# Kernel tuning notes

Measured on AMD Instinct MI355X. Metric: run time of the kernel, lower is better.

Reference implementation:

```python
import jax, jax.numpy as jnp
import numpy as np

DIM = 256
HEADS = 8
HEAD_DIM = DIM // HEADS
SR = 2
SCALE = HEAD_DIM ** -0.5
EPS = 1e-5
DN = ('NCHW', 'OIHW', 'NCHW')


def setup_inputs() -> dict:
    key = jax.random.key(0)
    ks = jax.random.split(key, 8)
    B, H, W = 4, 64, 64
    x = jax.random.normal(ks[0], (B, H * W, DIM), dtype=jnp.float32)
    # depthwise 3x3 convs (groups=dim): kernel [out_ch, 1, 3, 3]
    to_q_w = jax.random.normal(ks[1], (DIM, 1, 3, 3), dtype=jnp.float32) * 0.1
    to_kv_w = jax.random.normal(ks[2], (2 * DIM, 1, 3, 3), dtype=jnp.float32) * 0.1
    # spatial-reduction conv: kernel=stride=SR, with bias (torch Conv2d default)
    sr_w = jax.random.normal(ks[3], (DIM, DIM, SR, SR), dtype=jnp.float32) * 0.02
    sr_b = jax.random.normal(ks[4], (DIM,), dtype=jnp.float32) * 0.01
    ln_g = jnp.ones((DIM,), dtype=jnp.float32)
    ln_b = jnp.zeros((DIM,), dtype=jnp.float32)
    proj_w = jax.random.normal(ks[5], (DIM, DIM), dtype=jnp.float32) * 0.02
    proj_b = jax.random.normal(ks[6], (DIM,), dtype=jnp.float32) * 0.01
    return {
        'x': x, 'to_q_w': to_q_w, 'to_kv_w': to_kv_w,
        'sr_w': sr_w, 'sr_b': sr_b, 'ln_g': ln_g, 'ln_b': ln_b,
        'proj_w': proj_w, 'proj_b': proj_b, 'H': H, 'W': W,
    }


def reference(x, to_q_w, to_kv_w, sr_w, sr_b, ln_g, ln_b, proj_w, proj_b, H, W):
    B, N, C = x.shape
    x_nchw = x.reshape(B, H, W, C).transpose(0, 3, 1, 2)  # [B,C,H,W]

    # depthwise-conv Q projection (padding=1, stride=1 -> SAME)
    q = jax.lax.conv_general_dilated(x_nchw, to_q_w, (1, 1), 'SAME',
                                     feature_group_count=C, dimension_numbers=DN)
    q = q.transpose(0, 2, 3, 1).reshape(B, N, HEADS, HEAD_DIM).transpose(0, 2, 1, 3)  # [B,h,N,d]

    # spatial reduction: strided conv (kernel=stride=SR, no padding) + LayerNorm
    xr = jax.lax.conv_general_dilated(x_nchw, sr_w, (SR, SR), 'VALID',
                                      dimension_numbers=DN) + sr_b[None, :, None, None]
    Hs, Ws = xr.shape[2], xr.shape[3]
    Nk = Hs * Ws
    xr = xr.reshape(B, C, Nk).transpose(0, 2, 1)  # [B,Nk,C]
    mu = xr.mean(axis=-1, keepdims=True)
    var = ((xr - mu) ** 2).mean(axis=-1, keepdims=True)
    xr = (xr - mu) / jnp.sqrt(var + EPS) * ln_g + ln_b
    xr = xr.reshape(B, Hs, Ws, C).transpose(0, 3, 1, 2)  # [B,C,Hs,Ws]

    # depthwise-conv KV projection; torch group-major channel order out_ch=2*g+j
    kv = jax.lax.conv_general_dilated(xr, to_kv_w, (1, 1), 'SAME',
                                      feature_group_count=C, dimension_numbers=DN)
    kv = kv.transpose(0, 2, 3, 1).reshape(B, Nk, 2, HEADS, HEAD_DIM).transpose(2, 0, 3, 1, 4)
    k, v = kv[0], kv[1]  # [B,h,Nk,d]

    attn = jax.nn.softmax(jnp.einsum('bhqd,bhkd->bhqk', q, k) * SCALE, axis=-1)
    out = jnp.einsum('bhqk,bhkd->bhqd', attn, v)  # [B,h,N,d]
    out = out.transpose(0, 2, 1, 3).reshape(B, N, C)
    return out @ proj_w.T + proj_b
```

## Files before the change

kernel.cpp:

```cpp
#include <hip/hip_runtime.h>
#include <stdint.h>

typedef unsigned short u16;
typedef short s16x8 __attribute__((ext_vector_type(8)));
typedef short s16x4 __attribute__((ext_vector_type(4)));
typedef float f32x4 __attribute__((ext_vector_type(4)));
typedef uint32_t u32x4 __attribute__((ext_vector_type(4)));

#define SCALE 0.17677669529663689f
#define LOG2E 1.4426950408889634f
#define QS (SCALE * LOG2E)
#define EPS 1e-5f

static __device__ __forceinline__ float b2f(u16 u){
  union { uint32_t i; float f; } cv; cv.i = ((uint32_t)u) << 16; return cv.f;
}
static __device__ __forceinline__ u16 f2b(float f){
  uint32_t u = __float_as_uint(f);
  uint32_t r = (u + 0x7FFFu + ((u >> 16) & 1u)) >> 16;
  return (u16)r;
}
static __device__ __forceinline__ uint32_t cvtpk(float lo, float hi){
  uint32_t r;
  asm("v_cvt_pk_bf16_f32 %0, %1, %2" : "=v"(r) : "v"(lo), "v"(hi));
  return r;
}

__global__ __launch_bounds__(256) void k_prep(const float* __restrict__ x,
                                              const float* __restrict__ srw,
                                              const float* __restrict__ pw,
                                              u16* __restrict__ xbf,
                                              u16* __restrict__ wsr,
                                              u16* __restrict__ wpj){
  const int t = blockIdx.x*256 + threadIdx.x;
  if (t < 1048576){
    const float4 xv = ((const float4*)x)[t];
    ushort4 o;
    o.x = f2b(xv.x); o.y = f2b(xv.y); o.z = f2b(xv.z); o.w = f2b(xv.w);
    ((ushort4*)xbf)[t] = o;
  } else if (t < 1310720){
    const int t2 = t - 1048576;
    const int co = t2 >> 10, k = t2 & 1023;
    const float v = srw[(co<<10) + ((k&255)<<2) + (k>>8)];
    wsr[((((k>>3)<<8) + co)<<3) + (k&7)] = f2b(v);
  } else {
    const int t3 = t - 1310720;
    const int co = t3 >> 8, k = t3 & 255;
    wpj[((((k>>3)<<8) + co)<<3) + (k&7)] = f2b(pw[(co<<8) + k]);
  }
}

__global__ __launch_bounds__(256) void k_qconv(const u16* __restrict__ xbf,
                                               const float* __restrict__ w,
                                               u16* __restrict__ q){
  const int c = threadIdx.x;
  const int blk = blockIdx.x;
  const int b = blk >> 9;
  const int y = (blk >> 3) & 63;
  const int x0 = (blk & 7) << 3;
  float wv[9];
#pragma unroll
  for (int t = 0; t < 9; ++t) wv[t] = w[c*9 + t];
  float xin[3][10];
#pragma unroll
  for (int r = 0; r < 3; ++r){
    const int yy = y + r - 1;
    const bool yok = (unsigned)yy < 64u;
#pragma unroll
    for (int j = 0; j < 10; ++j){
      const int xx = x0 + j - 1;
      const bool ok = yok && ((unsigned)xx < 64u);
      xin[r][j] = ok ? b2f(xbf[(((b<<12) + (yy<<6) + xx) << 8) + c]) : 0.f;
    }
  }
#pragma unroll
  for (int j = 0; j < 8; ++j){
    float acc = 0.f;
#pragma unroll
    for (int r = 0; r < 3; ++r)
#pragma unroll
      for (int t = 0; t < 3; ++t)
        acc += xin[r][j+t] * wv[r*3 + t];
    q[(((b<<12) + (y<<6) + x0 + j) << 8) + c] = f2b(acc * QS);
  }
}

__global__ __launch_bounds__(256) void k_srgemm(const u16* __restrict__ xbf,
                                                const u16* __restrict__ wsr,
                                                const float* __restrict__ srb,
                                                const float* __restrict__ lng,
                                                const float* __restrict__ lnb,
                                                float* __restrict__ lnxr){
  __shared__ float red_s[16][4], red_q[16][4];
  __shared__ float mu_s[16], rs_s[16];
  const int tid = threadIdx.x;
  const int l = tid & 63, w = tid >> 6;
  const int r15 = l & 15, g = l >> 4;
  const int m0 = blockIdx.x << 4;
  const int ma = m0 + r15;
  const int bb_ = ma >> 10, nk = ma & 1023;
  const int hs = nk >> 5, wsx = nk & 31;
  int pixbase[4];
#pragma unroll
  for (int p = 0; p < 4; ++p){
    const int y = 2*hs + (p>>1), xx = 2*wsx + (p&1);
    pixbase[p] = (((bb_<<12) + (y<<6) + xx) << 8);
  }
  f32x4 acc[4];
#pragma unroll
  for (int i = 0; i < 4; ++i) acc[i] = (f32x4){0.f,0.f,0.f,0.f};
  for (int ks = 0; ks < 32; ++ks){
    const s16x8 af = *reinterpret_cast<const s16x8*>(
        xbf + pixbase[ks>>3] + ((ks&7)<<5) + (g<<3));
#pragma unroll
    for (int i = 0; i < 4; ++i){
      const int co = (((w<<2)+i)<<4) + r15;
      const s16x8 bf = *reinterpret_cast<const s16x8*>(
          wsr + (((((ks<<2)+g)<<8) + co)<<3));
      acc[i] = __builtin_amdgcn_mfma_f32_16x16x32_bf16(af, bf, acc[i], 0, 0, 0);
    }
  }
  float gv[4], bv[4];
#pragma unroll
  for (int i = 0; i < 4; ++i){
    const int co = (((w<<2)+i)<<4) + r15;
    const float sb = srb[co];
    gv[i] = lng[co]; bv[i] = lnb[co];
#pragma unroll
    for (int r = 0; r < 4; ++r) acc[i][r] += sb;
  }
  float s_r[4], q_r[4];
#pragma unroll
  for (int r = 0; r < 4; ++r){
    float s = 0.f, qq = 0.f;
#pragma unroll
    for (int i = 0; i < 4; ++i){ const float v = acc[i][r]; s += v; qq += v*v; }
#pragma unroll
    for (int off = 1; off < 16; off <<= 1){
      s  += __shfl_xor(s, off);
      qq += __shfl_xor(qq, off);
    }
    s_r[r] = s; q_r[r] = qq;
  }
  if (r15 == 0){
#pragma unroll
    for (int r = 0; r < 4; ++r){
      red_s[(g<<2)+r][w] = s_r[r];
      red_q[(g<<2)+r][w] = q_r[r];
    }
  }
  __syncthreads();
  if (tid < 16){
    const float s  = red_s[tid][0]+red_s[tid][1]+red_s[tid][2]+red_s[tid][3];
    const float qq = red_q[tid][0]+red_q[tid][1]+red_q[tid][2]+red_q[tid][3];
    const float mu = s * (1.f/256.f);
    mu_s[tid] = mu;
    rs_s[tid] = rsqrtf(qq*(1.f/256.f) - mu*mu + EPS);
  }
  __syncthreads();
  float mur[4], rsr[4];
#pragma unroll
  for (int r = 0; r < 4; ++r){ mur[r] = mu_s[(g<<2)+r]; rsr[r] = rs_s[(g<<2)+r]; }
#pragma unroll
  for (int i = 0; i < 4; ++i){
    const int co = (((w<<2)+i)<<4) + r15;
#pragma unroll
    for (int r = 0; r < 4; ++r)
      lnxr[(m0+(g<<2)+r)*256 + co] = (acc[i][r]-mur[r])*rsr[r]*gv[i] + bv[i];
  }
}

__global__ __launch_bounds__(512) void k_kvconv(const float* __restrict__ lnxr,
                                                const float* __restrict__ w,
                                                u16* __restrict__ kbuf,
                                                u16* __restrict__ vT){
  const int o = threadIdx.x;
  const int blk = blockIdx.x;
  const int b = blk >> 7;
  const int y = (blk >> 2) & 31;
  const int x0 = (blk & 3) << 3;
  const int g = o >> 1;
  float wv[9];
#pragma unroll
  for (int t = 0; t < 9; ++t) wv[t] = w[o*9 + t];
  float xin[3][10];
#pragma unroll
  for (int r = 0; r < 3; ++r){
    const int yy = y + r - 1;
    const bool yok = (unsigned)yy < 32u;
#pragma unroll
    for (int j = 0; j < 10; ++j){
      const int xx = x0 + j - 1;
      const bool ok = yok && ((unsigned)xx < 32u);
      xin[r][j] = ok ? lnxr[(((b<<10) + (yy<<5) + xx) << 8) + g] : 0.f;
    }
  }
  float acc[8];
#pragma unroll
  for (int j = 0; j < 8; ++j){
    float a = 0.f;
#pragma unroll
    for (int r = 0; r < 3; ++r)
#pragma unroll
      for (int t = 0; t < 3; ++t)
        a += xin[r][j+t] * wv[r*3 + t];
    acc[j] = a;
  }
  const int t = o & 255;
  const int h = t >> 5, dd = t & 31;
  if (o < 256){
    const int nkbase = (((b<<3) + h) << 10) + (y<<5) + x0;
#pragma unroll
    for (int j = 0; j < 8; ++j)
      kbuf[((nkbase + j) << 5) + dd] = f2b(acc[j]);
  } else {
    s16x8 pack;
#pragma unroll
    for (int j = 0; j < 8; ++j) pack[j] = (short)f2b(acc[j]);
    const int col0 = (y<<5) + x0;
    const int colS = (((col0>>3) ^ (dd&7)) << 3);
    *reinterpret_cast<s16x8*>(
        vT + (((((b<<3) + h) << 5) + dd) << 10) + colS) = pack;
  }
}

__global__ __launch_bounds__(512) void k_attn(const u16* __restrict__ q,
                                              const u16* __restrict__ kbuf,
                                              const u16* __restrict__ vT,
                                              u16* __restrict__ attb){
  __shared__ __align__(16) u16 KL[32768];
  __shared__ __align__(16) u16 VL[32768];
  const int tid = threadIdx.x;
  const int l = tid & 63, w = tid >> 6;
  const int i = blockIdx.x;
  const int xcd = i & 7, slot = i >> 3;
  const int bh = (xcd<<2) + (slot>>3);
  const int chunk = slot & 7;
  const int b = bh >> 3, h = bh & 7;
  const int r15 = l & 15, g = l >> 4;
  const int n0 = (chunk<<9) + (w<<6);

  {
    const uint4* kg = (const uint4*)(kbuf + (bh<<15));
    const uint4* vg = (const uint4*)(vT   + (bh<<15));
    uint4* kl = (uint4*)KL;
    uint4* vl = (uint4*)VL;
#pragma unroll
    for (int r = 0; r < 8; ++r){
      kl[(r<<9) + tid] = kg[(r<<9) + tid];
      vl[(r<<9) + tid] = vg[(r<<9) + tid];
    }
  }
  __syncthreads();

  s16x8 qf[4];
#pragma unroll
  for (int qi = 0; qi < 4; ++qi)
    qf[qi] = *reinterpret_cast<const s16x8*>(
        q + (((b<<12) + n0 + (qi<<4) + r15) << 8) + (h<<5) + (g<<3));

  f32x4 acc[4][2];
#pragma unroll
  for (int qi = 0; qi < 4; ++qi){
    acc[qi][0] = (f32x4){0.f,0.f,0.f,0.f};
    acc[qi][1] = (f32x4){0.f,0.f,0.f,0.f};
  }
  const f32x4 zero = {0.f,0.f,0.f,0.f};
  float lsum[4] = {0.f,0.f,0.f,0.f};
  const int vswz = (r15 & 7);

  for (int kv0 = 0; kv0 < 1024; kv0 += 64){
    s16x8 kf[4];
#pragma unroll
    for (int st = 0; st < 4; ++st)
      kf[st] = *reinterpret_cast<const s16x8*>(
          KL + ((kv0 + (st<<4) + r15) << 5) + (g<<3));
    s16x8 vf[2][2];
#pragma unroll
    for (int pr = 0; pr < 2; ++pr)
#pragma unroll
      for (int h2 = 0; h2 < 2; ++h2){
        const int cl  = kv0 + (pr<<5) + (g<<2);
        const int cl2 = cl + 16;
        const int rb  = ((h2<<4) + r15) << 10;
        const s16x4 v0 = *reinterpret_cast<const s16x4*>(
            VL + rb + (((cl >>3) ^ vswz) << 3) + (cl &7));
        const s16x4 v1 = *reinterpret_cast<const s16x4*>(
            VL + rb + (((cl2>>3) ^ vswz) << 3) + (cl2&7));
        s16x8 vv;
        vv[0]=v0[0]; vv[1]=v0[1]; vv[2]=v0[2]; vv[3]=v0[3];
        vv[4]=v1[0]; vv[5]=v1[1]; vv[6]=v1[2]; vv[7]=v1[3];
        vf[pr][h2] = vv;
      }
#pragma unroll
    for (int qi = 0; qi < 4; ++qi){
      f32x4 s[4];
      __builtin_amdgcn_s_setprio(1);
#pragma unroll
      for (int st = 0; st < 4; ++st)
        s[st] = __builtin_amdgcn_mfma_f32_16x16x32_bf16(kf[st], qf[qi], zero, 0, 0, 0);
      __builtin_amdgcn_s_setprio(0);
      float p[4][4];
      float ps = 0.f;
#pragma unroll
      for (int st = 0; st < 4; ++st)
#pragma unroll
        for (int r = 0; r < 4; ++r){
          const float e = __builtin_amdgcn_exp2f(s[st][r]);
          p[st][r] = e;
          ps += e;
        }
      ps += __shfl_xor(ps, 16);
      ps += __shfl_xor(ps, 32);
      lsum[qi] += ps;
      const u32x4 pk0 = {cvtpk(p[0][0],p[0][1]), cvtpk(p[0][2],p[0][3]),
                         cvtpk(p[1][0],p[1][1]), cvtpk(p[1][2],p[1][3])};
      const u32x4 pk1 = {cvtpk(p[2][0],p[2][1]), cvtpk(p[2][2],p[2][3]),
                         cvtpk(p[3][0],p[3][1]), cvtpk(p[3][2],p[3][3])};
      const s16x8 pf0 = __builtin_bit_cast(s16x8, pk0);
      const s16x8 pf1 = __builtin_bit_cast(s16x8, pk1);
      __builtin_amdgcn_s_setprio(1);
#pragma unroll
      for (int h2 = 0; h2 < 2; ++h2){
        acc[qi][h2] = __builtin_amdgcn_mfma_f32_16x16x32_bf16(pf0, vf[0][h2], acc[qi][h2], 0, 0, 0);
        acc[qi][h2] = __builtin_amdgcn_mfma_f32_16x16x32_bf16(pf1, vf[1][h2], acc[qi][h2], 0, 0, 0);
      }
      __builtin_amdgcn_s_setprio(0);
    }
  }
#pragma unroll
  for (int qi = 0; qi < 4; ++qi){
    const float linv = 1.f / lsum[qi];
#pragma unroll
    for (int r = 0; r < 4; ++r){
      const float fl = __shfl(linv, (g<<2) + r);
      const int n = n0 + (qi<<4) + (g<<2) + r;
      u16* orow = attb + (((b<<12) + n) << 8) + (h<<5) + r15;
      orow[0]  = f2b(acc[qi][0][r] * fl);
      orow[16] = f2b(acc[qi][1][r] * fl);
    }
  }
}

__global__ __launch_bounds__(256) void k_proj(const u16* __restrict__ attb,
                                              const u16* __restrict__ wpj,
                                              const float* __restrict__ pb,
                                              float* __restrict__ out){
  const int tid = threadIdx.x;
  const int l = tid & 63, w = tid >> 6;
  const int r15 = l & 15, g = l >> 4;
  const int m0 = blockIdx.x << 4;
  f32x4 acc[4];
#pragma unroll
  for (int i = 0; i < 4; ++i) acc[i] = (f32x4){0.f,0.f,0.f,0.f};
  const u16* arow = attb + (m0 + r15)*256 + (g<<3);
#pragma unroll
  for (int ks = 0; ks < 8; ++ks){
    const s16x8 af = *reinterpret_cast<const s16x8*>(arow + (ks<<5));
#pragma unroll
    for (int i = 0; i < 4; ++i){
      const int co = (((w<<2)+i)<<4) + r15;
      const s16x8 bf = *reinterpret_cast<const s16x8*>(
          wpj + (((((ks<<2)+g)<<8) + co)<<3));
      acc[i] = __builtin_amdgcn_mfma_f32_16x16x32_bf16(af, bf, acc[i], 0, 0, 0);
    }
  }
#pragma unroll
  for (int i = 0; i < 4; ++i){
    const int co = (((w<<2)+i)<<4) + r15;
    const float pbv = pb[co];
#pragma unroll
    for (int r = 0; r < 4; ++r)
      out[(m0+(g<<2)+r)*256 + co] = acc[i][r] + pbv;
  }
}

extern "C" void kernel_launch(void* const* d_in, const int* in_sizes, int n_in,
                              void* d_out, int out_size, void* d_ws, size_t ws_size,
                              hipStream_t stream){
  const float* x   = (const float*)d_in[0];
  const float* qw  = (const float*)d_in[1];
  const float* kvw = (const float*)d_in[2];
  const float* srw = (const float*)d_in[3];
  const float* srb = (const float*)d_in[4];
  const float* lng = (const float*)d_in[5];
  const float* lnb = (const float*)d_in[6];
  const float* pw  = (const float*)d_in[7];
  const float* pb  = (const float*)d_in[8];
  float* out = (float*)d_out;

  char* ws = (char*)d_ws;
  u16*   qbuf = (u16*)(ws);
  u16*   xbf  = (u16*)(ws + 8388608);
  u16*   attb = (u16*)(ws + 8388608);
  float* lnxr = (float*)(ws + 16777216);
  u16*   kbuf = (u16*)(ws + 20971520);
  u16*   vT   = (u16*)(ws + 23068672);
  u16*   wsr  = (u16*)(ws + 25165824);
  u16*   wpj  = (u16*)(ws + 25690112);

  hipLaunchKernelGGL(k_prep,   dim3(5376), dim3(256), 0, stream, x, srw, pw, xbf, wsr, wpj);
  hipLaunchKernelGGL(k_qconv,  dim3(2048), dim3(256), 0, stream, xbf, qw, qbuf);
  hipLaunchKernelGGL(k_srgemm, dim3(256),  dim3(256), 0, stream, xbf, wsr, srb, lng, lnb, lnxr);
  hipLaunchKernelGGL(k_kvconv, dim3(512),  dim3(512), 0, stream, lnxr, kvw, kbuf, vT);
  hipLaunchKernelGGL(k_attn,   dim3(256),  dim3(512), 0, stream, qbuf, kbuf, vT, attb);
  hipLaunchKernelGGL(k_proj,   dim3(1024), dim3(256), 0, stream, attb, wpj, pb, out);
}
```

Measured before the change: 86.83 us.

## Fuse x bf16 cast into qconv and give each wave full-row GEMM tiles

The fp32-to-bf16 conversion of x moves out of the prep kernel and into the depthwise Q conv, which now reads fp32 x directly and writes the bf16 copy as a side output. This removes one full pass over the input. The SR GEMM and projection GEMM now have each wave own 16 rows across all 256 output channels, so LayerNorm statistics reduce within a wave with no shared memory or barriers. The trade-offs are fewer blocks (64 and 256), more accumulator registers per wave, and qconv reading fp32, which doubles its load bytes.

Result: slower. 119.8 us (+37.9%).

```diff
diff --git a/kernel.cpp b/kernel.cpp
--- a/kernel.cpp
+++ b/kernel.cpp
@@ -12,9 +12,6 @@
 #define QS (SCALE * LOG2E)
 #define EPS 1e-5f
 
-static __device__ __forceinline__ float b2f(u16 u){
-  union { uint32_t i; float f; } cv; cv.i = ((uint32_t)u) << 16; return cv.f;
-}
 static __device__ __forceinline__ u16 f2b(float f){
   uint32_t u = __float_as_uint(f);
   uint32_t r = (u + 0x7FFFu + ((u >> 16) & 1u)) >> 16;
@@ -26,33 +23,26 @@
   return r;
 }
 
-__global__ __launch_bounds__(256) void k_prep(const float* __restrict__ x,
-                                              const float* __restrict__ srw,
+__global__ __launch_bounds__(256) void k_prep(const float* __restrict__ srw,
                                               const float* __restrict__ pw,
-                                              u16* __restrict__ xbf,
                                               u16* __restrict__ wsr,
                                               u16* __restrict__ wpj){
   const int t = blockIdx.x*256 + threadIdx.x;
-  if (t < 1048576){
-    const float4 xv = ((const float4*)x)[t];
-    ushort4 o;
-    o.x = f2b(xv.x); o.y = f2b(xv.y); o.z = f2b(xv.z); o.w = f2b(xv.w);
-    ((ushort4*)xbf)[t] = o;
-  } else if (t < 1310720){
-    const int t2 = t - 1048576;
-    const int co = t2 >> 10, k = t2 & 1023;
+  if (t < 262144){
+    const int co = t >> 10, k = t & 1023;
     const float v = srw[(co<<10) + ((k&255)<<2) + (k>>8)];
     wsr[((((k>>3)<<8) + co)<<3) + (k&7)] = f2b(v);
-  } else {
-    const int t3 = t - 1310720;
-    const int co = t3 >> 8, k = t3 & 255;
+  } else if (t < 327680){
+    const int u2 = t - 262144;
+    const int co = u2 >> 8, k = u2 & 255;
     wpj[((((k>>3)<<8) + co)<<3) + (k&7)] = f2b(pw[(co<<8) + k]);
   }
 }
 
-__global__ __launch_bounds__(256) void k_qconv(const u16* __restrict__ xbf,
+__global__ __launch_bounds__(256) void k_qconv(const float* __restrict__ x,
                                                const float* __restrict__ w,
-                                               u16* __restrict__ q){
+                                               u16* __restrict__ q,
+                                               u16* __restrict__ xbf){
   const int c = threadIdx.x;
   const int blk = blockIdx.x;
   const int b = blk >> 9;
@@ -70,7 +60,7 @@
     for (int j = 0; j < 10; ++j){
       const int xx = x0 + j - 1;
       const bool ok = yok && ((unsigned)xx < 64u);
-      xin[r][j] = ok ? b2f(xbf[(((b<<12) + (yy<<6) + xx) << 8) + c]) : 0.f;
+      xin[r][j] = ok ? x[(((b<<12) + (yy<<6) + xx) << 8) + c] : 0.f;
     }
   }
 #pragma unroll
@@ -81,7 +71,9 @@
 #pragma unroll
       for (int t = 0; t < 3; ++t)
         acc += xin[r][j+t] * wv[r*3 + t];
-    q[(((b<<12) + (y<<6) + x0 + j) << 8) + c] = f2b(acc * QS);
+    const int idx = (((b<<12) + (y<<6) + x0 + j) << 8) + c;
+    q[idx]   = f2b(acc * QS);
+    xbf[idx] = f2b(xin[1][j+1]);
   }
 }
 
@@ -91,12 +83,10 @@
                                                 const float* __restrict__ lng,
                                                 const float* __restrict__ lnb,
                                                 float* __restrict__ lnxr){
-  __shared__ float red_s[16][4], red_q[16][4];
-  __shared__ float mu_s[16], rs_s[16];
   const int tid = threadIdx.x;
   const int l = tid & 63, w = tid >> 6;
   const int r15 = l & 15, g = l >> 4;
-  const int m0 = blockIdx.x << 4;
+  const int m0 = (blockIdx.x << 6) + (w << 4);
   const int ma = m0 + r15;
   const int bb_ = ma >> 10, nk = ma & 1023;
   const int hs = nk >> 5, wsx = nk & 31;
@@ -106,67 +96,47 @@
     const int y = 2*hs + (p>>1), xx = 2*wsx + (p&1);
     pixbase[p] = (((bb_<<12) + (y<<6) + xx) << 8);
   }
-  f32x4 acc[4];
-#pragma unroll
-  for (int i = 0; i < 4; ++i) acc[i] = (f32x4){0.f,0.f,0.f,0.f};
+  f32x4 acc[16];
+#pragma unroll
+  for (int i = 0; i < 16; ++i) acc[i] = (f32x4){0.f,0.f,0.f,0.f};
   for (int ks = 0; ks < 32; ++ks){
     const s16x8 af = *reinterpret_cast<const s16x8*>(
         xbf + pixbase[ks>>3] + ((ks&7)<<5) + (g<<3));
 #pragma unroll
-    for (int i = 0; i < 4; ++i){
-      const int co = (((w<<2)+i)<<4) + r15;
+    for (int i = 0; i < 16; ++i){
       const s16x8 bf = *reinterpret_cast<const s16x8*>(
-          wsr + (((((ks<<2)+g)<<8) + co)<<3));
+          wsr + (((((ks<<2)+g)<<8) + (i<<4)+r15)<<3));
       acc[i] = __builtin_amdgcn_mfma_f32_16x16x32_bf16(af, bf, acc[i], 0, 0, 0);
     }
   }
-  float gv[4], bv[4];
-#pragma unroll
-  for (int i = 0; i < 4; ++i){
-    const int co = (((w<<2)+i)<<4) + r15;
-    const float sb = srb[co];
-    gv[i] = lng[co]; bv[i] = lnb[co];
+#pragma unroll
+  for (int i = 0; i < 16; ++i){
+    const float sb = srb[(i<<4)+r15];
 #pragma unroll
     for (int r = 0; r < 4; ++r) acc[i][r] += sb;
   }
-  float s_r[4], q_r[4];
+  float mu_r[4], rs_r[4];
 #pragma unroll
   for (int r = 0; r < 4; ++r){
     float s = 0.f, qq = 0.f;
 #pragma unroll
-    for (int i = 0; i < 4; ++i){ const float v = acc[i][r]; s += v; qq += v*v; }
+    for (int i = 0; i < 16; ++i){ const float v = acc[i][r]; s += v; qq += v*v; }
 #pragma unroll
     for (int off = 1; off < 16; off <<= 1){
       s  += __shfl_xor(s, off);
       qq += __shfl_xor(qq, off);
     }
-    s_r[r] = s; q_r[r] = qq;
-  }
-  if (r15 == 0){
-#pragma unroll
-    for (int r = 0; r < 4; ++r){
-      red_s[(g<<2)+r][w] = s_r[r];
-      red_q[(g<<2)+r][w] = q_r[r];
-    }
-  }
-  __syncthreads();
-  if (tid < 16){
-    const float s  = red_s[tid][0]+red_s[tid][1]+red_s[tid][2]+red_s[tid][3];
-    const float qq = red_q[tid][0]+red_q[tid][1]+red_q[tid][2]+red_q[tid][3];
     const float mu = s * (1.f/256.f);
-    mu_s[tid] = mu;
-    rs_s[tid] = rsqrtf(qq*(1.f/256.f) - mu*mu + EPS);
-  }
-  __syncthreads();
-  float mur[4], rsr[4];
-#pragma unroll
-  for (int r = 0; r < 4; ++r){ mur[r] = mu_s[(g<<2)+r]; rsr[r] = rs_s[(g<<2)+r]; }
-#pragma unroll
-  for (int i = 0; i < 4; ++i){
-    const int co = (((w<<2)+i)<<4) + r15;
+    mu_r[r] = mu;
+    rs_r[r] = rsqrtf(qq*(1.f/256.f) - mu*mu + EPS);
+  }
+#pragma unroll
+  for (int i = 0; i < 16; ++i){
+    const int co = (i<<4)+r15;
+    const float gv = lng[co], bv = lnb[co];
 #pragma unroll
     for (int r = 0; r < 4; ++r)
-      lnxr[(m0+(g<<2)+r)*256 + co] = (acc[i][r]-mur[r])*rsr[r]*gv[i] + bv[i];
+      lnxr[(m0+(g<<2)+r)*256 + co] = (acc[i][r]-mu_r[r])*rs_r[r]*gv + bv;
   }
 }
 
@@ -349,25 +319,24 @@
   const int tid = threadIdx.x;
   const int l = tid & 63, w = tid >> 6;
   const int r15 = l & 15, g = l >> 4;
-  const int m0 = blockIdx.x << 4;
-  f32x4 acc[4];
-#pragma unroll
-  for (int i = 0; i < 4; ++i) acc[i] = (f32x4){0.f,0.f,0.f,0.f};
+  const int m0 = (blockIdx.x << 6) + (w << 4);
+  f32x4 acc[16];
+#pragma unroll
+  for (int i = 0; i < 16; ++i) acc[i] = (f32x4){0.f,0.f,0.f,0.f};
   const u16* arow = attb + (m0 + r15)*256 + (g<<3);
 #pragma unroll
   for (int ks = 0; ks < 8; ++ks){
     const s16x8 af = *reinterpret_cast<const s16x8*>(arow + (ks<<5));
 #pragma unroll
-    for (int i = 0; i < 4; ++i){
-      const int co = (((w<<2)+i)<<4) + r15;
+    for (int i = 0; i < 16; ++i){
       const s16x8 bf = *reinterpret_cast<const s16x8*>(
-          wpj + (((((ks<<2)+g)<<8) + co)<<3));
+          wpj + (((((ks<<2)+g)<<8) + (i<<4)+r15)<<3));
       acc[i] = __builtin_amdgcn_mfma_f32_16x16x32_bf16(af, bf, acc[i], 0, 0, 0);
     }
   }
 #pragma unroll
-  for (int i = 0; i < 4; ++i){
-    const int co = (((w<<2)+i)<<4) + r15;
+  for (int i = 0; i < 16; ++i){
+    const int co = (i<<4)+r15;
     const float pbv = pb[co];
 #pragma unroll
     for (int r = 0; r < 4; ++r)
@@ -399,10 +368,10 @@
   u16*   wsr  = (u16*)(ws + 25165824);
   u16*   wpj  = (u16*)(ws + 25690112);
 
-  hipLaunchKernelGGL(k_prep,   dim3(5376), dim3(256), 0, stream, x, srw, pw, xbf, wsr, wpj);
-  hipLaunchKernelGGL(k_qconv,  dim3(2048), dim3(256), 0, stream, xbf, qw, qbuf);
-  hipLaunchKernelGGL(k_srgemm, dim3(256),  dim3(256), 0, stream, xbf, wsr, srb, lng, lnb, lnxr);
+  hipLaunchKernelGGL(k_prep,   dim3(1280), dim3(256), 0, stream, srw, pw, wsr, wpj);
+  hipLaunchKernelGGL(k_qconv,  dim3(2048), dim3(256), 0, stream, x, qw, qbuf, xbf);
+  hipLaunchKernelGGL(k_srgemm, dim3(64),   dim3(256), 0, stream, xbf, wsr, srb, lng, lnb, lnxr);
   hipLaunchKernelGGL(k_kvconv, dim3(512),  dim3(512), 0, stream, lnxr, kvw, kbuf, vT);
   hipLaunchKernelGGL(k_attn,   dim3(256),  dim3(512), 0, stream, qbuf, kbuf, vT, attb);
-  hipLaunchKernelGGL(k_proj,   dim3(1024), dim3(256), 0, stream, attb, wpj, pb, out);
-}
+  hipLaunchKernelGGL(k_proj,   dim3(256),  dim3(256), 0, stream, attb, wpj, pb, out);
+}
```
